# Optimization experiments

Measured on AMD Instinct MI355X. Metric: run time of the kernel, lower is better.

## Reference

```python
import jax, jax.numpy as jnp
import numpy as np

ALPHA = 0.2  # LeakyReLU negative slope
NEG_INF = -9e15

def leaky_relu(x):
    return jnp.where(x >= 0, x, ALPHA * x)

def setup_inputs() -> dict:
    key = jax.random.key(0)
    ks = jax.random.split(key, 7)
    B, N, D = 8, 1024, 256
    R = 12
    return {
        "h0": jax.random.normal(ks[0], (B, N, D), jnp.float32),
        "h1": jax.random.normal(ks[1], (B, N, D), jnp.float32),
        "multi_adj": jax.random.randint(ks[2], (R, B, N, N), 0, 2, jnp.int32),
        "adj": jax.random.randint(ks[3], (B, N, N), 0, 2, jnp.int32),
        "W": jax.random.normal(ks[4], (D, D), jnp.float32) * 0.05,
        "a": jax.random.normal(ks[5], (2 * D,), jnp.float32) * 0.05,
        "A_rel": jax.random.normal(ks[6], (R, 2 * D), jnp.float32) * 0.05,
    }

def reference(h0, h1, multi_adj, adj, W, a, A_rel):
    D = W.shape[1]
    Wh0 = jnp.einsum('bnd,de->bne', h0, W)  # [B,N0,D]
    Wh1 = jnp.einsum('bnd,de->bne', h1, W)  # [B,N1,D]
    # a_input @ v decomposes into outer-sum of per-node projections
    s0 = Wh0 @ a[:D]                         # [B,N0]
    s1 = Wh1 @ a[D:]                         # [B,N1]
    e = leaky_relu(s0[:, :, None] + s1[:, None, :])  # [B,N0,N1]
    attention = jnp.where(adj > 0, e, NEG_INF)
    # 12 relation score maps, fused: r0[r,b,i] + r1[r,b,j]
    r0 = jnp.einsum('bnd,rd->rbn', Wh0, A_rel[:, :D])  # [R,B,N0]
    r1 = jnp.einsum('bnd,rd->rbn', Wh1, A_rel[:, D:])  # [R,B,N1]
    e_rel = leaky_relu(r0[:, :, :, None] + r1[:, :, None, :])  # [R,B,N0,N1]
    rel_sum = jnp.where(multi_adj > 0, e_rel, 0.0).sum(axis=0)  # [B,N0,N1]
    # note: original softmax is over dim=1 (source-node axis N0)
    att = jax.nn.softmax(attention + 0.01 * rel_sum, axis=1)
    # dropout omitted (eval mode / deterministic baseline)
    h_prime = jnp.einsum('bij,bjd->bid', att, Wh1)
    return jax.nn.elu(h_prime)  # concat=True
```

## Files before the change

### kernel.cpp

```cpp
#include <hip/hip_runtime.h>
#include <hip/hip_bf16.h>
#include <hip/hip_fp16.h>

#define BB 8
#define NN 1024
#define DD 256
#define RR 12
#define BN (BB * NN)
#define ICH 8
#define CCH (NN / ICH)

typedef __attribute__((ext_vector_type(8))) short short8v;
typedef __attribute__((ext_vector_type(8))) _Float16 half8v;
typedef __attribute__((ext_vector_type(4))) float f32x4;
typedef __attribute__((ext_vector_type(4))) int int4v;

static __device__ __forceinline__ ushort f2bf(float f) {
  union { float f; uint u; } v; v.f = f;
  uint r = v.u + 0x7FFF + ((v.u >> 16) & 1);
  return (ushort)(r >> 16);
}
static __device__ __forceinline__ uint pack2(float a, float b) {
  return (uint)f2bf(a) | ((uint)f2bf(b) << 16);
}
static __device__ __forceinline__ ushort f2h(float f) {
  __half h = __float2half(f);
  union { __half h; ushort u; } v; v.h = h;
  return v.u;
}

__global__ __launch_bounds__(256) void k_prep(const float* __restrict__ W,
                                              const float* __restrict__ a,
                                              const float* __restrict__ A_rel,
                                              ushort* __restrict__ WTb,
                                              float* __restrict__ Vt) {
  __shared__ float Ls[64][65];
  int blk = blockIdx.x, tid = threadIdx.x;
  if (blk < 16) {
    int k0 = (blk & 3) * 64, d0 = (blk >> 2) * 64;
    int rr = tid >> 4, c = (tid & 15) * 4;
#pragma unroll
    for (int p = 0; p < 4; ++p) {
      int row = p * 16 + rr;
      float4 v = *(const float4*)&W[(k0 + row) * DD + d0 + c];
      Ls[row][c] = v.x; Ls[row][c + 1] = v.y; Ls[row][c + 2] = v.z; Ls[row][c + 3] = v.w;
    }
    __syncthreads();
    int r2 = tid >> 3, cc = (tid & 7) * 8;
#pragma unroll
    for (int p = 0; p < 2; ++p) {
      int d = p * 32 + r2;
      uint4 q;
      q.x = pack2(Ls[cc + 0][d], Ls[cc + 1][d]);
      q.y = pack2(Ls[cc + 2][d], Ls[cc + 3][d]);
      q.z = pack2(Ls[cc + 4][d], Ls[cc + 5][d]);
      q.w = pack2(Ls[cc + 6][d], Ls[cc + 7][d]);
      *(uint4*)&WTb[(d0 + d) * DD + k0 + cc] = q;
    }
  } else {
    int idx = blk - 16;
    int half = idx >= 26 ? 1 : 0;
    int c = idx - half * 26;
    if (c >= 13) return;
    int lane = tid & 63, w = tid >> 6;
    const float* X = (c == 0) ? &a[half * DD] : &A_rel[(c - 1) * 2 * DD + half * DD];
    float4 x4 = *(const float4*)&X[lane * 4];
    for (int kk = 0; kk < 64; ++kk) {
      int k = kk * 4 + w;
      float4 w4 = *(const float4*)&W[k * DD + lane * 4];
      float p = w4.x * x4.x + w4.y * x4.y + w4.z * x4.z + w4.w * x4.w;
#pragma unroll
      for (int off = 32; off; off >>= 1) p += __shfl_xor(p, off);
      if (lane == 0) Vt[(half * 13 + c) * DD + k] = p;
    }
  }
}

__global__ __launch_bounds__(256) void k_proj(const float* __restrict__ h0,
                                              const float* __restrict__ h1,
                                              const float* __restrict__ Vt,
                                              float* __restrict__ s0, float* __restrict__ s1,
                                              float* __restrict__ r0, float* __restrict__ r1) {
  int wid = (blockIdx.x * 256 + threadIdx.x) >> 6;
  int lane = threadIdx.x & 63;
  int mat = wid >> 13;
  int row = wid & (BN - 1);
  const float* h = mat ? h1 : h0;
  float4 h4 = *(const float4*)&h[(long)row * DD + lane * 4];
  float p[13];
#pragma unroll
  for (int c = 0; c < 13; ++c) {
    float4 v4 = *(const float4*)&Vt[(mat * 13 + c) * DD + lane * 4];
    p[c] = h4.x * v4.x + h4.y * v4.y + h4.z * v4.z + h4.w * v4.w;
  }
#pragma unroll
  for (int off = 32; off; off >>= 1)
#pragma unroll
    for (int c = 0; c < 13; ++c) p[c] += __shfl_xor(p[c], off);
  if (lane == 0) {
    if (mat == 0) {
      s0[row] = p[0];
      for (int c = 1; c < 13; ++c) r0[(c - 1) * BN + row] = p[c];
    } else {
      s1[row] = p[0];
      for (int c = 1; c < 13; ++c) r1[(c - 1) * BN + row] = p[c];
    }
  }
}

__global__ __launch_bounds__(256) void k_scores(const int* __restrict__ madj,
                                                const int* __restrict__ adj,
                                                const float* __restrict__ s0,
                                                const float* __restrict__ s1,
                                                const float* __restrict__ r0,
                                                const float* __restrict__ r1,
                                                ushort* __restrict__ U,
                                                float* __restrict__ psum) {
  int b = blockIdx.x, c = blockIdx.y;
  int tid = threadIdx.x;
  int j4 = tid * 4;
  int i0 = c * ICH;
  __shared__ float s0c[ICH];
  __shared__ float r0c[RR][ICH];
  if (tid < (RR + 1) * ICH) {
    int v = tid / ICH, i = tid % ICH;
    float x = (v == 0) ? s0[b * NN + i0 + i] : r0[(v - 1) * BN + b * NN + i0 + i];
    if (v == 0) s0c[i] = x; else r0c[v - 1][i] = x;
  }
  __syncthreads();
  float4 s14 = *(const float4*)&s1[b * NN + j4];
  float rel[ICH][4] = {};
#pragma unroll 1
  for (int r = 0; r < RR; ++r) {
    float4 r1v = *(const float4*)&r1[r * BN + b * NN + j4];
#pragma unroll
    for (int i = 0; i < ICH; ++i) {
      int4v mv = __builtin_nontemporal_load(
          (const int4v*)&madj[(((long)r * BB + b) * NN + i0 + i) * NN + j4]);
      float r0v = r0c[r][i];
      float t0 = r0v + r1v.x; t0 = t0 >= 0.f ? t0 : 0.2f * t0;
      float t1 = r0v + r1v.y; t1 = t1 >= 0.f ? t1 : 0.2f * t1;
      float t2 = r0v + r1v.z; t2 = t2 >= 0.f ? t2 : 0.2f * t2;
      float t3 = r0v + r1v.w; t3 = t3 >= 0.f ? t3 : 0.2f * t3;
      if (mv.x > 0) rel[i][0] += t0;
      if (mv.y > 0) rel[i][1] += t1;
      if (mv.z > 0) rel[i][2] += t2;
      if (mv.w > 0) rel[i][3] += t3;
    }
  }
  float l0 = 0.f, l1 = 0.f, l2 = 0.f, l3 = 0.f;
#pragma unroll
  for (int i = 0; i < ICH; ++i) {
    int4v av = __builtin_nontemporal_load(
        (const int4v*)&adj[((long)b * NN + i0 + i) * NN + j4]);
    float s0v = s0c[i];
    float u0, u1, u2, u3;
    { float e = s0v + s14.x; e = e >= 0.f ? e : 0.2f * e;
      u0 = __expf((av.x > 0 ? e : -9e15f) + 0.01f * rel[i][0] - 4.0f); }
    { float e = s0v + s14.y; e = e >= 0.f ? e : 0.2f * e;
      u1 = __expf((av.y > 0 ? e : -9e15f) + 0.01f * rel[i][1] - 4.0f); }
    { float e = s0v + s14.z; e = e >= 0.f ? e : 0.2f * e;
      u2 = __expf((av.z > 0 ? e : -9e15f) + 0.01f * rel[i][2] - 4.0f); }
    { float e = s0v + s14.w; e = e >= 0.f ? e : 0.2f * e;
      u3 = __expf((av.w > 0 ? e : -9e15f) + 0.01f * rel[i][3] - 4.0f); }
    uint2 so;
    so.x = (uint)f2h(u0) | ((uint)f2h(u1) << 16);
    so.y = (uint)f2h(u2) | ((uint)f2h(u3) << 16);
    *(uint2*)&U[((long)b * NN + i0 + i) * NN + j4] = so;
    l0 += u0; l1 += u1; l2 += u2; l3 += u3;
  }
  *(float4*)&psum[(long)c * BN + b * NN + j4] = make_float4(l0, l1, l2, l3);
}

__global__ __launch_bounds__(256) void k_mm_wh1(const float* __restrict__ h1,
                                                const ushort* __restrict__ WTb,
                                                ushort* __restrict__ WhT) {
  __shared__ __align__(16) char smraw[24576];
  uint4* AswQ = (uint4*)smraw;
  uint4* BswQ = (uint4*)(smraw + 8192);
  typedef ushort LtRow[72];
  LtRow* Lt = (LtRow*)smraw;
  int n0 = blockIdx.x * 128, i0 = blockIdx.y * 64;
  int tid = threadIdx.x;
  int r = tid >> 3, cs = tid & 7;
  int lane = tid & 63, wid = tid >> 6;
  int wm = wid >> 1, wn = wid & 1;
  int lr = lane & 15, g = lane >> 4;
  f32x4 acc[2][4] = {};
  for (int k0 = 0; k0 < DD; k0 += 64) {
#pragma unroll
    for (int p = 0; p < 2; ++p) {
      int row = p * 32 + r;
      const float* src = h1 + (long)(i0 + row) * DD + k0 + cs * 8;
      float4 v0 = *(const float4*)src;
      float4 v1 = *(const float4*)(src + 4);
      uint4 q;
      q.x = pack2(v0.x, v0.y); q.y = pack2(v0.z, v0.w);
      q.z = pack2(v1.x, v1.y); q.w = pack2(v1.z, v1.w);
      AswQ[row * 8 + (cs ^ (row & 7))] = q;
    }
#pragma unroll
    for (int p = 0; p < 4; ++p) {
      int row = p * 32 + r;
      uint4 q = *(const uint4*)(WTb + (long)(n0 + row) * DD + k0 + cs * 8);
      BswQ[row * 8 + (cs ^ (row & 7))] = q;
    }
    __syncthreads();
#pragma unroll
    for (int ks = 0; ks < 2; ++ks) {
      short8v af[2], bfr[4];
      int slot = ks * 4 + g;
#pragma unroll
      for (int mi = 0; mi < 2; ++mi) {
        int row = wm * 32 + mi * 16 + lr;
        af[mi] = *reinterpret_cast<const short8v*>(&AswQ[row * 8 + (slot ^ (row & 7))]);
      }
#pragma unroll
      for (int ni = 0; ni < 4; ++ni) {
        int row = wn * 64 + ni * 16 + lr;
        bfr[ni] = *reinterpret_cast<const short8v*>(&BswQ[row * 8 + (slot ^ (row & 7))]);
      }
#pragma unroll
      for (int mi = 0; mi < 2; ++mi)
#pragma unroll
        for (int ni = 0; ni < 4; ++ni)
          acc[mi][ni] = __builtin_amdgcn_mfma_f32_16x16x32_bf16(af[mi], bfr[ni], acc[mi][ni], 0, 0, 0);
    }
    __syncthreads();
  }
#pragma unroll
  for (int mi = 0; mi < 2; ++mi)
#pragma unroll
    for (int ni = 0; ni < 4; ++ni) {
      int d = wn * 64 + ni * 16 + lr;
      int ib = wm * 32 + mi * 16 + g * 4;
      uint2 w;
      w.x = pack2(acc[mi][ni][0], acc[mi][ni][1]);
      w.y = pack2(acc[mi][ni][2], acc[mi][ni][3]);
      *(uint2*)&Lt[d][ib] = w;
    }
  __syncthreads();
  int b = i0 >> 10, il = i0 & 1023;
#pragma unroll
  for (int p = 0; p < 4; ++p) {
    int row = (tid >> 3) + p * 32;
    int ch = (tid & 7) * 8;
    uint4 q = *(uint4*)&Lt[row][ch];
    *(uint4*)&WhT[((long)b * DD + n0 + row) * NN + il + ch] = q;
  }
}

__global__ __launch_bounds__(256) void k_combine(const float* __restrict__ psum,
                                                 float* __restrict__ li) {
  __shared__ float sm_l[256];
  int tid = threadIdx.x;
  int col_l = tid & 15, seg = tid >> 4;
  int col = blockIdx.x * 16 + col_l;
  float l = 0.f;
#pragma unroll
  for (int q = 0; q < 8; ++q) l += psum[(long)(seg * 8 + q) * BN + col];
  sm_l[tid] = l;
  __syncthreads();
  for (int s = 8; s; s >>= 1) {
    if (seg < s) sm_l[tid] += sm_l[tid + s * 16];
    __syncthreads();
  }
  if (seg == 0) li[col] = 1.0f / sm_l[tid];
}

__global__ __launch_bounds__(256) void k_av(const ushort* __restrict__ U,
                                            const float* __restrict__ li,
                                            const ushort* __restrict__ WhT,
                                            float* __restrict__ out) {
  __shared__ uint4 AswQ[64 * 8];
  __shared__ uint4 BswQ[128 * 8];
  int b = blockIdx.z;
  int i0 = blockIdx.y * 64;
  int n0 = blockIdx.x * 128;
  const ushort* Sb = U + (long)b * NN * NN;
  const ushort* Bb = WhT + (long)b * DD * NN;
  const float* lib = li + (long)b * NN;
  int tid = threadIdx.x;
  int r = tid >> 3, cs = tid & 7;
  int lane = tid & 63, wid = tid >> 6;
  int wm = wid >> 1, wn = wid & 1;
  int lr = lane & 15, g = lane >> 4;
  f32x4 acc[2][4] = {};
  for (int k0 = 0; k0 < NN; k0 += 64) {
#pragma unroll
    for (int p = 0; p < 2; ++p) {
      int row = p * 32 + r;
      uint4 sv = *(const uint4*)(Sb + (long)(i0 + row) * NN + k0 + cs * 8);
      half8v hv = *reinterpret_cast<const half8v*>(&sv);
      const float* lp = lib + k0 + cs * 8;
      float4 l0 = *(const float4*)lp, l1 = *(const float4*)(lp + 4);
      float v0 = (float)hv[0] * l0.x;
      float v1 = (float)hv[1] * l0.y;
      float v2 = (float)hv[2] * l0.z;
      float v3 = (float)hv[3] * l0.w;
      float v4 = (float)hv[4] * l1.x;
      float v5 = (float)hv[5] * l1.y;
      float v6 = (float)hv[6] * l1.z;
      float v7 = (float)hv[7] * l1.w;
      uint4 q;
      q.x = pack2(v0, v1); q.y = pack2(v2, v3);
      q.z = pack2(v4, v5); q.w = pack2(v6, v7);
      AswQ[row * 8 + (cs ^ (row & 7))] = q;
    }
#pragma unroll
    for (int p = 0; p < 4; ++p) {
      int row = p * 32 + r;
      uint4 q = *(const uint4*)(Bb + (long)(n0 + row) * NN + k0 + cs * 8);
      BswQ[row * 8 + (cs ^ (row & 7))] = q;
    }
    __syncthreads();
#pragma unroll
    for (int ks = 0; ks < 2; ++ks) {
      short8v af[2], bfr[4];
      int slot = ks * 4 + g;
#pragma unroll
      for (int mi = 0; mi < 2; ++mi) {
        int row = wm * 32 + mi * 16 + lr;
        af[mi] = *reinterpret_cast<const short8v*>(&AswQ[row * 8 + (slot ^ (row & 7))]);
      }
#pragma unroll
      for (int ni = 0; ni < 4; ++ni) {
        int row = wn * 64 + ni * 16 + lr;
        bfr[ni] = *reinterpret_cast<const short8v*>(&BswQ[row * 8 + (slot ^ (row & 7))]);
      }
#pragma unroll
      for (int mi = 0; mi < 2; ++mi)
#pragma unroll
        for (int ni = 0; ni < 4; ++ni)
          acc[mi][ni] = __builtin_amdgcn_mfma_f32_16x16x32_bf16(af[mi], bfr[ni], acc[mi][ni], 0, 0, 0);
    }
    __syncthreads();
  }
#pragma unroll
  for (int mi = 0; mi < 2; ++mi)
#pragma unroll
    for (int ni = 0; ni < 4; ++ni)
#pragma unroll
      for (int q = 0; q < 4; ++q) {
        int row = i0 + wm * 32 + mi * 16 + g * 4 + q;
        int col = n0 + wn * 64 + ni * 16 + lr;
        float x = acc[mi][ni][q];
        x = x > 0.f ? x : expm1f(x);
        out[((long)b * NN + row) * DD + col] = x;
      }
}

extern "C" void kernel_launch(void* const* d_in, const int* in_sizes, int n_in,
                              void* d_out, int out_size, void* d_ws, size_t ws_size,
                              hipStream_t stream) {
  const float* h0 = (const float*)d_in[0];
  const float* h1 = (const float*)d_in[1];
  const int* madj = (const int*)d_in[2];
  const int* adj = (const int*)d_in[3];
  const float* W = (const float*)d_in[4];
  const float* a = (const float*)d_in[5];
  const float* A_rel = (const float*)d_in[6];
  float* out = (float*)d_out;

  float* ws = (float*)d_ws;
  float* s0 = ws;
  float* s1 = s0 + BN;
  float* r0 = s1 + BN;
  float* r1 = r0 + RR * BN;
  float* psum = r1 + RR * BN;
  float* li = psum + (size_t)CCH * BN;
  float* Vt = li + BN;
  ushort* WTb = (ushort*)(Vt + 26 * DD);
  ushort* WhT = WTb + DD * DD;
  ushort* Uh = WhT + (size_t)BB * DD * NN;

  k_prep<<<68, 256, 0, stream>>>(W, a, A_rel, WTb, Vt);
  k_proj<<<(2 * BN) / 4, 256, 0, stream>>>(h0, h1, Vt, s0, s1, r0, r1);
  k_scores<<<dim3(BB, CCH), 256, 0, stream>>>(madj, adj, s0, s1, r0, r1, Uh, psum);
  k_mm_wh1<<<dim3(2, BN / 64), 256, 0, stream>>>(h1, WTb, WhT);
  k_combine<<<512, 256, 0, stream>>>(psum, li);
  k_av<<<dim3(2, NN / 64, BB), 256, 0, stream>>>(Uh, li, WhT, out);
}
```

Measured before the change: 171.0 us.

## Fold softmax normalization into Wh1 rows and store unnormalized scores as bf16

The score kernel now writes bf16 exponentials with nontemporal stores and accumulates column sums with atomics into a zeroed buffer, which replaces the partial-sum array and the separate combine kernel. The reciprocal column sum is applied to rows of Wh1 in the projection GEMM epilogue instead of to the score matrix. That lets the attention GEMM load U straight into shared memory with no per-element fp16 convert, multiply and repack. This removes one launch, the psum traffic and the conversion work in the main GEMM loop. In exchange it adds an extra memset, atomic contention on BN floats, and lower-precision bf16 probabilities.

Measured after the change: 175.2 us. +2.4%, slower.

```diff
diff --git a/kernel.cpp b/kernel.cpp
--- a/kernel.cpp
+++ b/kernel.cpp
@@ -11,9 +11,9 @@
 #define CCH (NN / ICH)
 
 typedef __attribute__((ext_vector_type(8))) short short8v;
-typedef __attribute__((ext_vector_type(8))) _Float16 half8v;
 typedef __attribute__((ext_vector_type(4))) float f32x4;
 typedef __attribute__((ext_vector_type(4))) int int4v;
+typedef __attribute__((ext_vector_type(2))) uint uint2v;
 
 static __device__ __forceinline__ ushort f2bf(float f) {
   union { float f; uint u; } v; v.f = f;
@@ -23,10 +23,9 @@
 static __device__ __forceinline__ uint pack2(float a, float b) {
   return (uint)f2bf(a) | ((uint)f2bf(b) << 16);
 }
-static __device__ __forceinline__ ushort f2h(float f) {
-  __half h = __float2half(f);
-  union { __half h; ushort u; } v; v.h = h;
-  return v.u;
+static __device__ __forceinline__ float bfround(float f) {
+  union { uint u; float f; } v; v.u = (uint)f2bf(f) << 16;
+  return v.f;
 }
 
 __global__ __launch_bounds__(256) void k_prep(const float* __restrict__ W,
@@ -115,7 +114,7 @@
                                                 const float* __restrict__ r0,
                                                 const float* __restrict__ r1,
                                                 ushort* __restrict__ U,
-                                                float* __restrict__ psum) {
+                                                float* __restrict__ lsum) {
   int b = blockIdx.x, c = blockIdx.y;
   int tid = threadIdx.x;
   int j4 = tid * 4;
@@ -163,17 +162,23 @@
       u2 = __expf((av.z > 0 ? e : -9e15f) + 0.01f * rel[i][2] - 4.0f); }
     { float e = s0v + s14.w; e = e >= 0.f ? e : 0.2f * e;
       u3 = __expf((av.w > 0 ? e : -9e15f) + 0.01f * rel[i][3] - 4.0f); }
-    uint2 so;
-    so.x = (uint)f2h(u0) | ((uint)f2h(u1) << 16);
-    so.y = (uint)f2h(u2) | ((uint)f2h(u3) << 16);
-    *(uint2*)&U[((long)b * NN + i0 + i) * NN + j4] = so;
+    u0 = bfround(u0); u1 = bfround(u1); u2 = bfround(u2); u3 = bfround(u3);
+    uint2v so;
+    so.x = pack2(u0, u1);
+    so.y = pack2(u2, u3);
+    __builtin_nontemporal_store(so, (uint2v*)&U[((long)b * NN + i0 + i) * NN + j4]);
     l0 += u0; l1 += u1; l2 += u2; l3 += u3;
   }
-  *(float4*)&psum[(long)c * BN + b * NN + j4] = make_float4(l0, l1, l2, l3);
+  float* lp = &lsum[b * NN + j4];
+  atomicAdd(lp + 0, l0);
+  atomicAdd(lp + 1, l1);
+  atomicAdd(lp + 2, l2);
+  atomicAdd(lp + 3, l3);
 }
 
 __global__ __launch_bounds__(256) void k_mm_wh1(const float* __restrict__ h1,
                                                 const ushort* __restrict__ WTb,
+                                                const float* __restrict__ lsum,
                                                 ushort* __restrict__ WhT) {
   __shared__ __align__(16) char smraw[24576];
   uint4* AswQ = (uint4*)smraw;
@@ -229,16 +234,19 @@
     __syncthreads();
   }
 #pragma unroll
-  for (int mi = 0; mi < 2; ++mi)
+  for (int mi = 0; mi < 2; ++mi) {
+    int ib = wm * 32 + mi * 16 + g * 4;
+    float4 lv = *(const float4*)&lsum[i0 + ib];
+    float inv0 = 1.0f / lv.x, inv1 = 1.0f / lv.y, inv2 = 1.0f / lv.z, inv3 = 1.0f / lv.w;
 #pragma unroll
     for (int ni = 0; ni < 4; ++ni) {
       int d = wn * 64 + ni * 16 + lr;
-      int ib = wm * 32 + mi * 16 + g * 4;
       uint2 w;
-      w.x = pack2(acc[mi][ni][0], acc[mi][ni][1]);
-      w.y = pack2(acc[mi][ni][2], acc[mi][ni][3]);
+      w.x = pack2(acc[mi][ni][0] * inv0, acc[mi][ni][1] * inv1);
+      w.y = pack2(acc[mi][ni][2] * inv2, acc[mi][ni][3] * inv3);
       *(uint2*)&Lt[d][ib] = w;
     }
+  }
   __syncthreads();
   int b = i0 >> 10, il = i0 & 1023;
 #pragma unroll
@@ -250,26 +258,7 @@
   }
 }
 
-__global__ __launch_bounds__(256) void k_combine(const float* __restrict__ psum,
-                                                 float* __restrict__ li) {
-  __shared__ float sm_l[256];
-  int tid = threadIdx.x;
-  int col_l = tid & 15, seg = tid >> 4;
-  int col = blockIdx.x * 16 + col_l;
-  float l = 0.f;
-#pragma unroll
-  for (int q = 0; q < 8; ++q) l += psum[(long)(seg * 8 + q) * BN + col];
-  sm_l[tid] = l;
-  __syncthreads();
-  for (int s = 8; s; s >>= 1) {
-    if (seg < s) sm_l[tid] += sm_l[tid + s * 16];
-    __syncthreads();
-  }
-  if (seg == 0) li[col] = 1.0f / sm_l[tid];
-}
-
 __global__ __launch_bounds__(256) void k_av(const ushort* __restrict__ U,
-                                            const float* __restrict__ li,
                                             const ushort* __restrict__ WhT,
                                             float* __restrict__ out) {
   __shared__ uint4 AswQ[64 * 8];
@@ -279,7 +268,6 @@
   int n0 = blockIdx.x * 128;
   const ushort* Sb = U + (long)b * NN * NN;
   const ushort* Bb = WhT + (long)b * DD * NN;
-  const float* lib = li + (long)b * NN;
   int tid = threadIdx.x;
   int r = tid >> 3, cs = tid & 7;
   int lane = tid & 63, wid = tid >> 6;
@@ -290,28 +278,14 @@
 #pragma unroll
     for (int p = 0; p < 2; ++p) {
       int row = p * 32 + r;
-      uint4 sv = *(const uint4*)(Sb + (long)(i0 + row) * NN + k0 + cs * 8);
-      half8v hv = *reinterpret_cast<const half8v*>(&sv);
-      const float* lp = lib + k0 + cs * 8;
-      float4 l0 = *(const float4*)lp, l1 = *(const float4*)(lp + 4);
-      float v0 = (float)hv[0] * l0.x;
-      float v1 = (float)hv[1] * l0.y;
-      float v2 = (float)hv[2] * l0.z;
-      float v3 = (float)hv[3] * l0.w;
-      float v4 = (float)hv[4] * l1.x;
-      float v5 = (float)hv[5] * l1.y;
-      float v6 = (float)hv[6] * l1.z;
-      float v7 = (float)hv[7] * l1.w;
-      uint4 q;
-      q.x = pack2(v0, v1); q.y = pack2(v2, v3);
-      q.z = pack2(v4, v5); q.w = pack2(v6, v7);
-      AswQ[row * 8 + (cs ^ (row & 7))] = q;
+      AswQ[row * 8 + (cs ^ (row & 7))] =
+          *(const uint4*)(Sb + (long)(i0 + row) * NN + k0 + cs * 8);
     }
 #pragma unroll
     for (int p = 0; p < 4; ++p) {
       int row = p * 32 + r;
-      uint4 q = *(const uint4*)(Bb + (long)(n0 + row) * NN + k0 + cs * 8);
-      BswQ[row * 8 + (cs ^ (row & 7))] = q;
+      BswQ[row * 8 + (cs ^ (row & 7))] =
+          *(const uint4*)(Bb + (long)(n0 + row) * NN + k0 + cs * 8);
     }
     __syncthreads();
 #pragma unroll
@@ -367,17 +341,16 @@
   float* s1 = s0 + BN;
   float* r0 = s1 + BN;
   float* r1 = r0 + RR * BN;
-  float* psum = r1 + RR * BN;
-  float* li = psum + (size_t)CCH * BN;
-  float* Vt = li + BN;
+  float* lsum = r1 + RR * BN;
+  float* Vt = lsum + BN;
   ushort* WTb = (ushort*)(Vt + 26 * DD);
   ushort* WhT = WTb + DD * DD;
   ushort* Uh = WhT + (size_t)BB * DD * NN;
 
+  hipMemsetAsync(lsum, 0, BN * sizeof(float), stream);
   k_prep<<<68, 256, 0, stream>>>(W, a, A_rel, WTb, Vt);
   k_proj<<<(2 * BN) / 4, 256, 0, stream>>>(h0, h1, Vt, s0, s1, r0, r1);
-  k_scores<<<dim3(BB, CCH), 256, 0, stream>>>(madj, adj, s0, s1, r0, r1, Uh, psum);
-  k_mm_wh1<<<dim3(2, BN / 64), 256, 0, stream>>>(h1, WTb, WhT);
-  k_combine<<<512, 256, 0, stream>>>(psum, li);
-  k_av<<<dim3(2, NN / 64, BB), 256, 0, stream>>>(Uh, li, WhT, out);
-}
+  k_scores<<<dim3(BB, CCH), 256, 0, stream>>>(madj, adj, s0, s1, r0, r1, Uh, lsum);
+  k_mm_wh1<<<dim3(2, BN / 64), 256, 0, stream>>>(h1, WTb, lsum, WhT);
+  k_av<<<dim3(2, NN / 64, BB), 256, 0, stream>>>(Uh, WhT, out);
+}
```
